# Performance work log

Measured on AMD Instinct MI355X. Metric: run time of the kernel, lower is better.

Reference implementation:

```python
import jax, jax.numpy as jnp
import numpy as np

B, T, TB, TV, TR = 4, 512, 512, 512, 256
D, H = 1024, 16
HD = D // H
D4 = D // 4
DFF = 4096
ROPE_THETA = 10000.0


def _rms(x, w, eps=1e-6):
    return x * jax.lax.rsqrt(jnp.mean(x * x, -1, keepdims=True) + eps) * w


def _ln(x, w, b, eps=1e-5):
    m = jnp.mean(x, -1, keepdims=True)
    v = jnp.var(x, -1, keepdims=True)
    return (x - m) * jax.lax.rsqrt(v + eps) * w + b


def _rope_cs(L, hd):
    inv = 1.0 / (ROPE_THETA ** (jnp.arange(0, hd, 2, dtype=jnp.float32) / hd))
    f = jnp.arange(L, dtype=jnp.float32)[:, None] * inv[None, :]
    e = jnp.concatenate([f, f], -1)  # (L, hd)
    return jnp.cos(e), jnp.sin(e)


def _rot_half(x):
    h = x.shape[-1] // 2
    return jnp.concatenate([-x[..., h:], x[..., :h]], -1)


def _rope(x, cos, sin):
    return x * cos + _rot_half(x) * sin


def _heads(x):
    b, l, _ = x.shape
    return x.reshape(b, l, H, HD).transpose(0, 2, 1, 3)  # (B,H,L,hd)


def setup_inputs() -> dict:
    key = jax.random.key(0)
    ks = jax.random.split(key, 16)
    def n(k, shape, s=0.02):
        return jax.random.normal(k, shape, jnp.float32) * s
    return {
        'x': n(ks[0], (B, T, D), 1.0),
        'bev_tokens': n(ks[1], (B, TB, D), 1.0),
        'vl_tokens': n(ks[2], (B, TV, D), 1.0),
        'reasoning_tokens': n(ks[3], (B, TR, D), 1.0),
        'conditioning': n(ks[4], (B, D), 1.0),
        'ln_pre_w': jnp.ones((D,)), 'ln_pre_b': jnp.zeros((D,)),
        'adaln_w': n(ks[5], (6 * D, D)), 'adaln_b': jnp.zeros((6 * D,)),
        'q_proj_w': n(ks[6], (D, D)), 'q_proj_b': jnp.zeros((D,)),
        'qa_w': n(ks[7], (3, D4, D)), 'qa_b': jnp.zeros((3, D4)),
        'qa_out_w': n(ks[8], (D, D4)), 'qa_out_b': jnp.zeros((D,)),
        'k_w': n(ks[9], (4, D, D)), 'k_b': jnp.zeros((4, D)),
        'v_w': n(ks[10], (4, D, D)), 'v_b': jnp.zeros((4, D)),
        'o_w': n(ks[11], (D, D)), 'o_b': jnp.zeros((D,)),
        'qn_w': jnp.ones((HD,)), 'kn_w': jnp.ones((HD,)),
        'gating': jnp.full((1,), 0.5, jnp.float32),
        'temps': jnp.zeros((4,)), 'score_biases': jnp.zeros((4,)),
        'ffn_ln_w': jnp.ones((D,)), 'ffn_ln_b': jnp.zeros((D,)),
        'ffn_w1': n(ks[12], (DFF, D)), 'ffn_b1': jnp.zeros((DFF,)),
        'ffn_w2': n(ks[13], (D, DFF)), 'ffn_b2': jnp.zeros((D,)),
    }


def reference(x, bev_tokens, vl_tokens, reasoning_tokens, conditioning,
              ln_pre_w, ln_pre_b, adaln_w, adaln_b,
              q_proj_w, q_proj_b, qa_w, qa_b, qa_out_w, qa_out_b,
              k_w, k_b, v_w, v_b, o_w, o_b, qn_w, kn_w,
              gating, temps, score_biases,
              ffn_ln_w, ffn_ln_b, ffn_w1, ffn_b1, ffn_w2, ffn_b2):
    # AdaLN modulation (T_route == 0 path: single modulation for whole sequence)
    mod = jax.nn.silu(conditioning) @ adaln_w.T + adaln_b  # (B, 6D)
    shift_pre, scale_pre, gate_attn, shift_ffn, scale_ffn, gate_ffn = jnp.split(mod, 6, axis=1)
    x_norm = _ln(x, ln_pre_w, ln_pre_b) * (1.0 + scale_pre[:, None, :]) + shift_pre[:, None, :]

    # Self Q and per-source K/V (sources: self, bev, vl, reasoning)
    q_self = _heads(x_norm @ q_proj_w.T + q_proj_b)
    srcs = [x_norm, bev_tokens, vl_tokens, reasoning_tokens]
    k_all = [_heads(s @ k_w[i].T + k_b[i]) for i, s in enumerate(srcs)]
    v_all = [_heads(s @ v_w[i].T + v_b[i]) for i, s in enumerate(srcs)]

    # Source-specific adapter queries: d -> d/4 -> d (shared out proj)
    q_ad = [_heads((x_norm @ qa_w[i].T + qa_b[i]) @ qa_out_w.T + qa_out_b) for i in range(3)]

    # QK-Norm (RMSNorm on head_dim)
    q_all = [_rms(q, qn_w) for q in [q_self] + q_ad]
    k_all = [_rms(k, kn_w) for k in k_all]

    # RoPE: Q and K for self-attention; K only for cross sources
    cosT, sinT = _rope_cs(x.shape[1], HD)
    q_all[0] = _rope(q_all[0], cosT, sinT)
    k_roped = []
    for k in k_all:
        c, s = _rope_cs(k.shape[2], HD)
        k_roped.append(_rope(k, c, s))

    # Per-source temperature / bias; gating only on reasoning scores
    temp = 1.0 + jax.nn.softplus(temps)
    ratio_g = jnp.tanh(gating[0])
    inv_sqrt_d = HD ** -0.5
    scores = []
    for i in range(4):
        s = jnp.einsum('bhqd,bhkd->bhqk', q_all[i], k_roped[i]) * (inv_sqrt_d * temp[i]) + score_biases[i]
        if i == 3:
            s = s * ratio_g
        scores.append(s)

    attn = jax.nn.softmax(jnp.concatenate(scores, -1), axis=-1)  # joint softmax
    v_cat = jnp.concatenate(v_all, 2)  # (B,H,T+TB+TV+TR,hd)
    out = jnp.einsum('bhqk,bhkd->bhqd', attn, v_cat)
    out = out.transpose(0, 2, 1, 3).reshape(x.shape) @ o_w.T + o_b
    x = x + gate_attn[:, None, :] * out

    # FFN with AdaLN modulation (dropout = identity at eval)
    h = _ln(x, ffn_ln_w, ffn_ln_b) * (1.0 + scale_ffn[:, None, :]) + shift_ffn[:, None, :]
    h = jax.nn.gelu(h @ ffn_w1.T + ffn_b1, approximate=False) @ ffn_w2.T + ffn_b2
    return x + gate_ffn[:, None, :] * h
```

## Files before the change

### kernel.cpp

```cpp
#include <hip/hip_runtime.h>

typedef unsigned short ushort_t;
typedef __attribute__((ext_vector_type(8))) __bf16 bf16x8;
typedef __attribute__((ext_vector_type(4))) float f32x4;

__device__ __forceinline__ float bf2f(ushort_t u) {
    union { unsigned int i; float f; } v; v.i = ((unsigned int)u) << 16; return v.f;
}
__device__ __forceinline__ ushort_t f2bf(float f) {
    union { float f; unsigned int i; } v; v.f = f;
    unsigned int r = (v.i + 0x7FFFu + ((v.i >> 16) & 1u)) >> 16;
    return (ushort_t)r;
}
__device__ __forceinline__ float gelu_exact(float v) {
    return 0.5f * v * (1.f + erff(v * 0.70710678118654752f));
}
__device__ __forceinline__ float ld1(const void* p, size_t i, int isf32) {
    return isf32 ? ((const float*)p)[i] : bf2f(((const ushort_t*)p)[i]);
}
__device__ __forceinline__ void stage8(const void* p, size_t idx, int isf32, ushort_t* dst) {
    if (isf32) {
        const float* f = (const float*)p + idx;
        float4 u = *(const float4*)f;
        float4 v = *(const float4*)(f + 4);
        dst[0] = f2bf(u.x); dst[1] = f2bf(u.y); dst[2] = f2bf(u.z); dst[3] = f2bf(u.w);
        dst[4] = f2bf(v.x); dst[5] = f2bf(v.y); dst[6] = f2bf(v.z); dst[7] = f2bf(v.w);
    } else {
        *(uint4*)dst = *(const uint4*)((const ushort_t*)p + idx);
    }
}
__device__ __forceinline__ void gload16(const ushort_t* g, ushort_t* l) {
    __builtin_amdgcn_global_load_lds(
        (const __attribute__((address_space(1))) unsigned int*)g,
        (__attribute__((address_space(3))) unsigned int*)l, 16, 0, 0);
}

__device__ __forceinline__ void store_q(ushort_t* qbuf, int row, int c, int p0, float v) {
    int b = row >> 9, t = row & 511;
    qbuf[((((size_t)(b * 16 + (c >> 6))) * 4 + p0) * 512 + t) * 64 + (c & 63)] = f2bf(v);
}
__device__ __forceinline__ void store_k(ushort_t* kbuf, int row, int c, int koff, int p1, float v) {
    int b = row >> p1, t = row & ((1 << p1) - 1);
    kbuf[(((size_t)(b * 16 + (c >> 6))) * 1792 + koff + t) * 64 + (c & 63)] = f2bf(v);
}
__device__ __forceinline__ void store_v(ushort_t* vbufT, int row, int c, int koff, int p1, float v) {
    int b = row >> p1, t = row & ((1 << p1) - 1);
    vbufT[(((size_t)(b * 16 + (c >> 6))) * 64 + (c & 63)) * 1792 + koff + t] = f2bf(v);
}

__global__ void detect_kernel(const unsigned int* __restrict__ x, int* __restrict__ flag) {
    if (threadIdx.x == 0 && blockIdx.x == 0) {
        int sane = 0;
        for (int i = 0; i < 256; i++) {
            unsigned int e = (x[i] >> 7) & 0xFFu;
            if (e == 0u || (e >= 100u && e <= 140u)) sane++;
        }
        *flag = (sane >= 200) ? 0 : 1;
    }
}

static constexpr size_t CV_ADALN = 0;
static constexpr size_t CV_QPROJ = 6291456;
static constexpr size_t CV_QA    = 7340032;
static constexpr size_t CV_QAOUT = 8126464;
static constexpr size_t CV_KW    = 8388608;
static constexpr size_t CV_VW    = 12582912;
static constexpr size_t CV_OW    = 16777216;
static constexpr size_t CV_FFN1  = 17825792;
static constexpr size_t CV_FFN2  = 22020096;
static constexpr size_t CV_TOTAL = 26214400;

__global__ void __launch_bounds__(256) convert_weights_kernel(
    const void* s0, const void* s1, const void* s2, const void* s3,
    const void* s4, const void* s5, const void* s6, const void* s7,
    const void* s8, ushort_t* __restrict__ dst, const int* __restrict__ dflag) {
    int isf32 = *dflag;
    size_t i8 = ((size_t)blockIdx.x * 256 + threadIdx.x) * 8;
    if (i8 >= CV_TOTAL) return;
    const void* src; size_t base;
    if      (i8 < CV_QPROJ) { src = s0; base = CV_ADALN; }
    else if (i8 < CV_QA)    { src = s1; base = CV_QPROJ; }
    else if (i8 < CV_QAOUT) { src = s2; base = CV_QA; }
    else if (i8 < CV_KW)    { src = s3; base = CV_QAOUT; }
    else if (i8 < CV_VW)    { src = s4; base = CV_KW; }
    else if (i8 < CV_OW)    { src = s5; base = CV_VW; }
    else if (i8 < CV_FFN1)  { src = s6; base = CV_OW; }
    else if (i8 < CV_FFN2)  { src = s7; base = CV_FFN1; }
    else                    { src = s8; base = CV_FFN2; }
    ushort_t t8[8];
    stage8(src, i8 - base, isf32, t8);
    *(uint4*)(dst + i8) = *(uint4*)t8;
}

__global__ void __launch_bounds__(256) convert_act_kernel(
    const void* __restrict__ src, ushort_t* __restrict__ dst, int n8,
    const int* __restrict__ dflag) {
    int c8 = blockIdx.x * 256 + threadIdx.x;
    if (c8 >= n8) return;
    int isf32 = *dflag;
    size_t i8 = (size_t)c8 * 8;
    ushort_t t8[8];
    stage8(src, i8, isf32, t8);
    *(uint4*)(dst + i8) = *(uint4*)t8;
}

__global__ void prep_consts_kernel(const void* __restrict__ temps,
                                   const void* __restrict__ biases,
                                   const void* __restrict__ gating,
                                   float* __restrict__ consts,
                                   const int* __restrict__ dflag) {
    if (threadIdx.x == 0 && blockIdx.x == 0) {
        int isf32 = *dflag;
        float g = tanhf(ld1(gating, 0, isf32));
        for (int s = 0; s < 4; s++) {
            float t  = ld1(temps, s, isf32);
            float sp = (t > 20.f) ? t : log1pf(expf(t));
            float scale = 0.125f * (1.f + sp);
            float mul = (s == 3) ? g : 1.f;
            consts[s]     = scale * mul;
            consts[4 + s] = ld1(biases, s, isf32) * mul;
        }
    }
}

__global__ void __launch_bounds__(256) adaln_kernel(
    const void* __restrict__ cond, const void* __restrict__ w,
    const void* __restrict__ bias, float* __restrict__ mod,
    int wmode, const int* __restrict__ dflag) {
    __shared__ float cs[1024];
    int isf32 = *dflag;
    int wf = (wmode == 2) ? 0 : isf32;
    int b = blockIdx.y, tid = threadIdx.x;
    for (int i = tid; i < 1024; i += 256) {
        float c = ld1(cond, b * 1024 + i, isf32);
        cs[i] = c / (1.f + expf(-c));
    }
    __syncthreads();
    int n = blockIdx.x * 256 + tid;
    float acc = 0.f;
    if (wf) {
        const float* wr = (const float*)w + (size_t)n * 1024;
        for (int d = 0; d < 1024; d += 8) {
            float4 a = *(const float4*)(wr + d);
            float4 bb = *(const float4*)(wr + d + 4);
            acc += cs[d+0]*a.x + cs[d+1]*a.y + cs[d+2]*a.z + cs[d+3]*a.w
                 + cs[d+4]*bb.x + cs[d+5]*bb.y + cs[d+6]*bb.z + cs[d+7]*bb.w;
        }
    } else {
        const ushort_t* wr = (const ushort_t*)w + (size_t)n * 1024;
        for (int d = 0; d < 1024; d += 8) {
            uint4 raw = *(const uint4*)(wr + d);
            const ushort_t* u = (const ushort_t*)&raw;
            acc += cs[d+0]*bf2f(u[0]) + cs[d+1]*bf2f(u[1]) + cs[d+2]*bf2f(u[2]) + cs[d+3]*bf2f(u[3])
                 + cs[d+4]*bf2f(u[4]) + cs[d+5]*bf2f(u[5]) + cs[d+6]*bf2f(u[6]) + cs[d+7]*bf2f(u[7]);
        }
    }
    mod[(size_t)b * 6144 + n] = acc + ld1(bias, n, isf32);
}

template <int SRC>
__global__ void __launch_bounds__(256) ln_mod_kernel(
    const void* __restrict__ xin, const float* __restrict__ mod,
    const void* __restrict__ lnw, const void* __restrict__ lnb,
    int shift_off, int scale_off, ushort_t* __restrict__ out,
    const int* __restrict__ dflag) {
    int isf32 = *dflag;
    int row = blockIdx.x, tid = threadIdx.x;
    int b = row >> 9;
    float v[4];
    #pragma unroll
    for (int i = 0; i < 4; i++) {
        size_t idx = (size_t)row * 1024 + tid + 256 * i;
        v[i] = (SRC == 1) ? ((const float*)xin)[idx] : ld1(xin, idx, isf32);
    }
    float s = v[0] + v[1] + v[2] + v[3];
    float ss = v[0]*v[0] + v[1]*v[1] + v[2]*v[2] + v[3]*v[3];
    #pragma unroll
    for (int off = 1; off < 64; off <<= 1) {
        s  += __shfl_xor(s,  off, 64);
        ss += __shfl_xor(ss, off, 64);
    }
    __shared__ float red[8];
    int w = tid >> 6;
    if ((tid & 63) == 0) { red[w] = s; red[4 + w] = ss; }
    __syncthreads();
    s  = red[0] + red[1] + red[2] + red[3];
    ss = red[4] + red[5] + red[6] + red[7];
    float mean = s * (1.f / 1024.f);
    float var  = ss * (1.f / 1024.f) - mean * mean;
    float inv  = rsqrtf(var + 1e-5f);
    const float* mb = mod + (size_t)b * 6144;
    #pragma unroll
    for (int i = 0; i < 4; i++) {
        int d = tid + 256 * i;
        float xn = (v[i] - mean) * inv;
        float y  = xn * ld1(lnw, d, isf32) + ld1(lnb, d, isf32);
        out[(size_t)row * 1024 + d] = f2bf(y * (1.f + mb[scale_off + d]) + mb[shift_off + d]);
    }
}

template <int EPI>
__global__ void __launch_bounds__(256) gemm_bt_kernel(
    const void* __restrict__ A, int lda,
    const void* __restrict__ W, int wrow0,
    const void* __restrict__ bias,
    void* __restrict__ Cout, int ldc, int K, int p0, int p1,
    int a_ext, int wmode, const int* __restrict__ dflag) {
    __shared__ ushort_t As[64][40];
    __shared__ ushort_t Bs[64][40];
    int isf32 = *dflag;
    int fa = a_ext ? isf32 : 0;
    int fw = (wmode == 2) ? 0 : isf32;
    int m0 = blockIdx.x * 64, n0 = blockIdx.y * 64;
    int tid = threadIdx.x;
    int r = tid >> 2, c = (tid & 3) * 8;
    int w = tid >> 6, ln = tid & 63;
    int msub = (w & 1) * 32, nsub = (w >> 1) * 32;
    int fr = ln & 15, q = ln >> 4;
    f32x4 acc00 = {0.f,0.f,0.f,0.f}, acc01 = {0.f,0.f,0.f,0.f};
    f32x4 acc10 = {0.f,0.f,0.f,0.f}, acc11 = {0.f,0.f,0.f,0.f};
    for (int k0 = 0; k0 < K; k0 += 32) {
        __syncthreads();
        {
            ushort_t t8[8];
            stage8(A, (size_t)(m0 + r) * lda + c + k0, fa, t8);
            *(uint4*)&As[r][c] = *(uint4*)t8;
        }
        {
            ushort_t t8[8];
            stage8(W, (size_t)(wrow0 + n0 + r) * K + c + k0, fw, t8);
            *(uint4*)&Bs[r][c] = *(uint4*)t8;
        }
        __syncthreads();
        bf16x8 a0 = *(const bf16x8*)&As[msub + fr][q * 8];
        bf16x8 a1 = *(const bf16x8*)&As[msub + 16 + fr][q * 8];
        bf16x8 b0 = *(const bf16x8*)&Bs[nsub + fr][q * 8];
        bf16x8 b1 = *(const bf16x8*)&Bs[nsub + 16 + fr][q * 8];
        acc00 = __builtin_amdgcn_mfma_f32_16x16x32_bf16(a0, b0, acc00, 0, 0, 0);
        acc01 = __builtin_amdgcn_mfma_f32_16x16x32_bf16(a0, b1, acc01, 0, 0, 0);
        acc10 = __builtin_amdgcn_mfma_f32_16x16x32_bf16(a1, b0, acc10, 0, 0, 0);
        acc11 = __builtin_amdgcn_mfma_f32_16x16x32_bf16(a1, b1, acc11, 0, 0, 0);
    }
    int col0 = n0 + nsub + fr;
    float bv0 = ld1(bias, wrow0 + col0, isf32);
    float bv1 = ld1(bias, wrow0 + col0 + 16, isf32);
    #pragma unroll
    for (int mi = 0; mi < 2; mi++) {
        #pragma unroll
        for (int ni = 0; ni < 2; ni++) {
            f32x4 a = (mi == 0) ? (ni == 0 ? acc00 : acc01) : (ni == 0 ? acc10 : acc11);
            int col = col0 + ni * 16;
            float bb = (ni == 0) ? bv0 : bv1;
            #pragma unroll
            for (int e = 0; e < 4; e++) {
                int rowg = m0 + msub + mi * 16 + q * 4 + e;
                float v = a[e] + bb;
                if (EPI == 2) v = gelu_exact(v);
                if (EPI == 0) {
                    ((float*)Cout)[(size_t)rowg * ldc + col] = v;
                } else if (EPI == 1 || EPI == 2) {
                    ((ushort_t*)Cout)[(size_t)rowg * ldc + col] = f2bf(v);
                } else if (EPI == 3) {
                    store_k((ushort_t*)Cout, rowg, col, p0, p1, v);
                } else if (EPI == 5) {
                    store_v((ushort_t*)Cout, rowg, col, p0, p1, v);
                } else {
                    store_q((ushort_t*)Cout, rowg, col, p0, v);
                }
            }
        }
    }
}

__device__ __forceinline__ void gemm_mainloop(
    const ushort_t* __restrict__ A, int lda,
    const ushort_t* __restrict__ W, int ldw,
    int m0, int wrow0, int kbeg, int klen,
    ushort_t* As, ushort_t* Bs, f32x4 acc[4][4])
{
    const int tid = threadIdx.x;
    const int w = tid >> 6;
    const int ln = tid & 63;
    const int fr = ln & 15, q = ln >> 4;
    const int wm = w & 1, wn = w >> 1;
    const ushort_t* gA = A + (size_t)(m0 + (tid >> 2)) * lda + kbeg + (tid & 3) * 8;
    const ushort_t* gW = W + (size_t)(wrow0 + (tid >> 2)) * ldw + kbeg + (tid & 3) * 8;
    const size_t sA = (size_t)64 * lda;
    const size_t sW = (size_t)64 * ldw;
    ushort_t* lA = As + w * 512;
    ushort_t* lB = Bs + w * 512;
    for (int k = 0; k < klen; k += 32) {
        __syncthreads();
        gload16(gA, lA);
        gload16(gA + sA, lA + 2048);
        gload16(gW, lB);
        gload16(gW + sW, lB + 2048);
        gA += 32; gW += 32;
        __syncthreads();
        bf16x8 af[4], bfr[4];
        #pragma unroll
        for (int mi = 0; mi < 4; mi++)
            af[mi] = *(const bf16x8*)&As[(wm * 64 + mi * 16 + fr) * 32 + q * 8];
        #pragma unroll
        for (int ni = 0; ni < 4; ni++)
            bfr[ni] = *(const bf16x8*)&Bs[(wn * 64 + ni * 16 + fr) * 32 + q * 8];
        #pragma unroll
        for (int mi = 0; mi < 4; mi++)
            #pragma unroll
            for (int ni = 0; ni < 4; ni++)
                acc[mi][ni] = __builtin_amdgcn_mfma_f32_16x16x32_bf16(af[mi], bfr[ni], acc[mi][ni], 0, 0, 0);
    }
}

__global__ void __launch_bounds__(256) gemm_qkvqa_kernel(
    const ushort_t* __restrict__ xnorm,
    const ushort_t* __restrict__ Wq, const ushort_t* __restrict__ Wqa,
    const ushort_t* __restrict__ Wk, const ushort_t* __restrict__ Wv,
    const void* __restrict__ bq, const void* __restrict__ bqa,
    const void* __restrict__ bk, const void* __restrict__ bv,
    ushort_t* __restrict__ qbuf, ushort_t* __restrict__ qah,
    ushort_t* __restrict__ kbuf, ushort_t* __restrict__ vbufT,
    const int* __restrict__ dflag)
{
    __shared__ ushort_t As[4096], Bs[4096];
    int isf32 = *dflag;
    int m0 = blockIdx.x * 128, n0 = blockIdx.y * 128;
    int seg, wrow0;
    const ushort_t* W; const void* bias;
    if (n0 < 1024)      { seg = 0; W = Wq;  bias = bq;  wrow0 = n0; }
    else if (n0 < 1792) { seg = 1; W = Wqa; bias = bqa; wrow0 = n0 - 1024; }
    else if (n0 < 2816) { seg = 2; W = Wk;  bias = bk;  wrow0 = n0 - 1792; }
    else                { seg = 3; W = Wv;  bias = bv;  wrow0 = n0 - 2816; }
    f32x4 acc[4][4];
    #pragma unroll
    for (int i = 0; i < 4; i++)
        #pragma unroll
        for (int j = 0; j < 4; j++) acc[i][j] = (f32x4){0.f, 0.f, 0.f, 0.f};
    gemm_mainloop(xnorm, 1024, W, 1024, m0, wrow0, 0, 1024, As, Bs, acc);
    int tid = threadIdx.x, w = tid >> 6, ln = tid & 63;
    int fr = ln & 15, q = ln >> 4, wm = w & 1, wn = w >> 1;
    #pragma unroll
    for (int ni = 0; ni < 4; ni++) {
        int c = wrow0 + wn * 64 + ni * 16 + fr;
        float bb = ld1(bias, c, isf32);
        #pragma unroll
        for (int mi = 0; mi < 4; mi++) {
            #pragma unroll
            for (int e = 0; e < 4; e++) {
                int row = m0 + wm * 64 + mi * 16 + q * 4 + e;
                float v = acc[mi][ni][e] + bb;
                if (seg == 0)      store_q(qbuf, row, c, 0, v);
                else if (seg == 1) qah[(size_t)row * 768 + c] = f2bf(v);
                else if (seg == 2) store_k(kbuf, row, c, 0, 9, v);
                else               store_v(vbufT, row, c, 0, 9, v);
            }
        }
    }
}

__global__ void __launch_bounds__(256) gemm_kv_kernel(
    const ushort_t* __restrict__ A,
    const ushort_t* __restrict__ Wk, const ushort_t* __restrict__ Wv,
    const void* __restrict__ kb, const void* __restrict__ vb, int boff,
    ushort_t* __restrict__ kbuf, ushort_t* __restrict__ vbufT,
    int koff, int p1, const int* __restrict__ dflag)
{
    __shared__ ushort_t As[4096], Bs[4096];
    int isf32 = *dflag;
    int m0 = blockIdx.x * 128, n0 = blockIdx.y * 128;
    int isK = (n0 < 1024);
    int wrow0 = isK ? n0 : n0 - 1024;
    const ushort_t* W = isK ? Wk : Wv;
    const void* bias = isK ? kb : vb;
    f32x4 acc[4][4];
    #pragma unroll
    for (int i = 0; i < 4; i++)
        #pragma unroll
        for (int j = 0; j < 4; j++) acc[i][j] = (f32x4){0.f, 0.f, 0.f, 0.f};
    gemm_mainloop(A, 1024, W, 1024, m0, wrow0, 0, 1024, As, Bs, acc);
    int tid = threadIdx.x, w = tid >> 6, ln = tid & 63;
    int fr = ln & 15, q = ln >> 4, wm = w & 1, wn = w >> 1;
    #pragma unroll
    for (int ni = 0; ni < 4; ni++) {
        int c = wrow0 + wn * 64 + ni * 16 + fr;
        float bb = ld1(bias, boff + c, isf32);
        #pragma unroll
        for (int mi = 0; mi < 4; mi++) {
            #pragma unroll
            for (int e = 0; e < 4; e++) {
                int row = m0 + wm * 64 + mi * 16 + q * 4 + e;
                float v = acc[mi][ni][e] + bb;
                if (isK) store_k(kbuf, row, c, koff, p1, v);
                else     store_v(vbufT, row, c, koff, p1, v);
            }
        }
    }
}

__global__ void __launch_bounds__(256) gemm_qaout_kernel(
    const ushort_t* __restrict__ qah,
    const ushort_t* __restrict__ W, const void* __restrict__ bias,
    ushort_t* __restrict__ qbuf, const int* __restrict__ dflag)
{
    __shared__ ushort_t As[4096], Bs[4096];
    int isf32 = *dflag;
    int m0 = blockIdx.x * 128, n0 = blockIdx.y * 128;
    int z = blockIdx.z;
    const ushort_t* A = qah + (size_t)z * 256;
    f32x4 acc[4][4];
    #pragma unroll
    for (int i = 0; i < 4; i++)
        #pragma unroll
        for (int j = 0; j < 4; j++) acc[i][j] = (f32x4){0.f, 0.f, 0.f, 0.f};
    gemm_mainloop(A, 768, W, 256, m0, n0, 0, 256, As, Bs, acc);
    int tid = threadIdx.x, w = tid >> 6, ln = tid & 63;
    int fr = ln & 15, q = ln >> 4, wm = w & 1, wn = w >> 1;
    #pragma unroll
    for (int ni = 0; ni < 4; ni++) {
        int c = n0 + wn * 64 + ni * 16 + fr;
        float bb = ld1(bias, c, isf32);
        #pragma unroll
        for (int mi = 0; mi < 4; mi++) {
            #pragma unroll
            for (int e = 0; e < 4; e++) {
                int row = m0 + wm * 64 + mi * 16 + q * 4 + e;
                store_q(qbuf, row, c, 1 + z, acc[mi][ni][e] + bb);
            }
        }
    }
}

template <int EPI>
__global__ void __launch_bounds__(256) gemm_plain_kernel(
    const ushort_t* __restrict__ A, int lda,
    const ushort_t* __restrict__ W, int ldw,
    const void* __restrict__ bias,
    void* __restrict__ Cout, int ldc, int ksub, size_t zstride,
    const int* __restrict__ dflag)
{
    __shared__ ushort_t As[4096], Bs[4096];
    int isf32 = *dflag;
    int m0 = blockIdx.x * 128, n0 = blockIdx.y * 128;
    int z = blockIdx.z;
    f32x4 acc[4][4];
    #pragma unroll
    for (int i = 0; i < 4; i++)
        #pragma unroll
        for (int j = 0; j < 4; j++) acc[i][j] = (f32x4){0.f, 0.f, 0.f, 0.f};
    gemm_mainloop(A, lda, W, ldw, m0, n0, z * ksub, ksub, As, Bs, acc);
    int tid = threadIdx.x, w = tid >> 6, ln = tid & 63;
    int fr = ln & 15, q = ln >> 4, wm = w & 1, wn = w >> 1;
    #pragma unroll
    for (int ni = 0; ni < 4; ni++) {
        int c = n0 + wn * 64 + ni * 16 + fr;
        float bb = (z == 0) ? ld1(bias, c, isf32) : 0.f;
        #pragma unroll
        for (int mi = 0; mi < 4; mi++) {
            #pragma unroll
            for (int e = 0; e < 4; e++) {
                int row = m0 + wm * 64 + mi * 16 + q * 4 + e;
                float v = acc[mi][ni][e] + bb;
                if (EPI == 2) {
                    ((ushort_t*)Cout)[(size_t)row * ldc + c] = f2bf(gelu_exact(v));
                } else {
                    ((float*)Cout)[z * zstride + (size_t)row * ldc + c] = v;
                }
            }
        }
    }
}

__global__ void __launch_bounds__(256) qrope_ip_kernel(
    ushort_t* __restrict__ qbuf, const void* __restrict__ qnw,
    const int* __restrict__ dflag) {
    int isf32 = *dflag;
    int w = threadIdx.x >> 6, ln = threadIdx.x & 63;
    int flat = blockIdx.x * 4 + w;
    int t = flat & 511, s = (flat >> 9) & 3;
    ushort_t* p = qbuf + (size_t)flat * 64;
    float x = bf2f(p[ln]);
    float ssum = x * x;
    #pragma unroll
    for (int off = 1; off < 64; off <<= 1) ssum += __shfl_xor(ssum, off, 64);
    float y = x * rsqrtf(ssum * (1.f / 64.f) + 1e-6f) * ld1(qnw, ln, isf32);
    if (s == 0) {
        float ang = (float)t * expf(-(float)(ln & 31) * (9.210340371976184f / 32.f));
        float cs, sn;
        sincosf(ang, &sn, &cs);
        float other = __shfl_xor(y, 32, 64);
        y = y * cs + ((ln < 32) ? -other : other) * sn;
    }
    p[ln] = f2bf(y);
}

__global__ void __launch_bounds__(256) krope_ip_kernel(
    ushort_t* __restrict__ kbuf, const void* __restrict__ knw,
    const int* __restrict__ dflag) {
    int isf32 = *dflag;
    int w = threadIdx.x >> 6, ln = threadIdx.x & 63;
    int flat = blockIdx.x * 4 + w;
    int j = flat % 1792;
    int t = j & 511;
    ushort_t* p = kbuf + (size_t)flat * 64;
    float x = bf2f(p[ln]);
    float ssum = x * x;
    #pragma unroll
    for (int off = 1; off < 64; off <<= 1) ssum += __shfl_xor(ssum, off, 64);
    float y = x * rsqrtf(ssum * (1.f / 64.f) + 1e-6f) * ld1(knw, ln, isf32);
    float ang = (float)t * expf(-(float)(ln & 31) * (9.210340371976184f / 32.f));
    float cs, sn;
    sincosf(ang, &sn, &cs);
    float other = __shfl_xor(y, 32, 64);
    y = y * cs + ((ln < 32) ? -other : other) * sn;
    p[ln] = f2bf(y);
}

__global__ void __launch_bounds__(256) attn_mfma_kernel(
    const ushort_t* __restrict__ qbuf, const ushort_t* __restrict__ kbuf,
    const ushort_t* __restrict__ vbufT, const float* __restrict__ consts,
    ushort_t* __restrict__ attn_out) {
    __shared__ ushort_t ks[2][64][72];
    __shared__ ushort_t vsT[2][64][72];
    __shared__ ushort_t ps[4][16][72];
    int bh = blockIdx.y;
    int b = bh >> 4, h = bh & 15;
    int tid = threadIdx.x, w = tid >> 6, ln = tid & 63;
    int r0 = blockIdx.x * 64 + w * 16;
    int m = ln & 15, quad = ln >> 4;

    const ushort_t* qb = qbuf + (size_t)bh * 4 * 512 * 64;
    bf16x8 qf00 = *(const bf16x8*)(qb + ((size_t)(0 * 512 + r0 + m)) * 64 + quad * 8);
    bf16x8 qf01 = *(const bf16x8*)(qb + ((size_t)(0 * 512 + r0 + m)) * 64 + 32 + quad * 8);
    bf16x8 qf10 = *(const bf16x8*)(qb + ((size_t)(1 * 512 + r0 + m)) * 64 + quad * 8);
    bf16x8 qf11 = *(const bf16x8*)(qb + ((size_t)(1 * 512 + r0 + m)) * 64 + 32 + quad * 8);
    bf16x8 qf20 = *(const bf16x8*)(qb + ((size_t)(2 * 512 + r0 + m)) * 64 + quad * 8);
    bf16x8 qf21 = *(const bf16x8*)(qb + ((size_t)(2 * 512 + r0 + m)) * 64 + 32 + quad * 8);
    bf16x8 qf30 = *(const bf16x8*)(qb + ((size_t)(3 * 512 + r0 + m)) * 64 + quad * 8);
    bf16x8 qf31 = *(const bf16x8*)(qb + ((size_t)(3 * 512 + r0 + m)) * 64 + 32 + quad * 8);

    float m_i[4], l_i[4];
    f32x4 acc[4];
    #pragma unroll
    for (int e = 0; e < 4; e++) { m_i[e] = -1e30f; l_i[e] = 0.f; }
    #pragma unroll
    for (int d = 0; d < 4; d++) acc[d] = (f32x4){0.f, 0.f, 0.f, 0.f};

    const ushort_t* kb  = kbuf  + (size_t)bh * 1792 * 64;
    const ushort_t* vbT = vbufT + (size_t)bh * 64 * 1792;
    int skey = tid >> 3, sd = (tid & 7) * 8;
    uint4 kreg0 = *(const uint4*)(kb + (size_t)skey * 64 + sd);
    uint4 kreg1 = *(const uint4*)(kb + (size_t)(skey + 32) * 64 + sd);
    uint4 vreg0 = *(const uint4*)(vbT + (size_t)skey * 1792 + sd);
    uint4 vreg1 = *(const uint4*)(vbT + (size_t)(skey + 32) * 1792 + sd);
    *(uint4*)&ks[0][skey][sd]       = kreg0;
    *(uint4*)&ks[0][skey + 32][sd]  = kreg1;
    *(uint4*)&vsT[0][skey][sd]      = vreg0;
    *(uint4*)&vsT[0][skey + 32][sd] = vreg1;
    __syncthreads();
    int tcnt = 0, p = 0;

    #pragma unroll
    for (int s = 0; s < 4; s++) {
        const float a_s = consts[s];
        const float b_s = consts[4 + s];
        const bf16x8 qA0 = (s == 0) ? qf00 : (s == 1) ? qf10 : (s == 2) ? qf20 : qf30;
        const bf16x8 qA1 = (s == 0) ? qf01 : (s == 1) ? qf11 : (s == 2) ? qf21 : qf31;
        const int NT = (s == 3) ? 4 : 8;
        for (int ti = 0; ti < NT; ti++) {
            if (tcnt < 27) {
                int nx = (tcnt + 1) * 64;
                kreg0 = *(const uint4*)(kb + (size_t)(nx + skey) * 64 + sd);
                kreg1 = *(const uint4*)(kb + (size_t)(nx + skey + 32) * 64 + sd);
                vreg0 = *(const uint4*)(vbT + (size_t)skey * 1792 + nx + sd);
                vreg1 = *(const uint4*)(vbT + (size_t)(skey + 32) * 1792 + nx + sd);
            }
            f32x4 zero = {0.f, 0.f, 0.f, 0.f};
            bf16x8 k0a = *(const bf16x8*)&ks[p][m][quad * 8];
            bf16x8 k0b = *(const bf16x8*)&ks[p][m][32 + quad * 8];
            bf16x8 k1a = *(const bf16x8*)&ks[p][16 + m][quad * 8];
            bf16x8 k1b = *(const bf16x8*)&ks[p][16 + m][32 + quad * 8];
            bf16x8 k2a = *(const bf16x8*)&ks[p][32 + m][quad * 8];
            bf16x8 k2b = *(const bf16x8*)&ks[p][32 + m][32 + quad * 8];
            bf16x8 k3a = *(const bf16x8*)&ks[p][48 + m][quad * 8];
            bf16x8 k3b = *(const bf16x8*)&ks[p][48 + m][32 + quad * 8];
            f32x4 sc0 = __builtin_amdgcn_mfma_f32_16x16x32_bf16(qA0, k0a, zero, 0, 0, 0);
            sc0 = __builtin_amdgcn_mfma_f32_16x16x32_bf16(qA1, k0b, sc0, 0, 0, 0);
            f32x4 sc1 = __builtin_amdgcn_mfma_f32_16x16x32_bf16(qA0, k1a, zero, 0, 0, 0);
            sc1 = __builtin_amdgcn_mfma_f32_16x16x32_bf16(qA1, k1b, sc1, 0, 0, 0);
            f32x4 sc2 = __builtin_amdgcn_mfma_f32_16x16x32_bf16(qA0, k2a, zero, 0, 0, 0);
            sc2 = __builtin_amdgcn_mfma_f32_16x16x32_bf16(qA1, k2b, sc2, 0, 0, 0);
            f32x4 sc3 = __builtin_amdgcn_mfma_f32_16x16x32_bf16(qA0, k3a, zero, 0, 0, 0);
            sc3 = __builtin_amdgcn_mfma_f32_16x16x32_bf16(qA1, k3b, sc3, 0, 0, 0);
            #pragma unroll
            for (int e = 0; e < 4; e++) {
                float s0 = sc0[e] * a_s + b_s;
                float s1 = sc1[e] * a_s + b_s;
                float s2 = sc2[e] * a_s + b_s;
                float s3 = sc3[e] * a_s + b_s;
                float mxe = fmaxf(fmaxf(s0, s1), fmaxf(s2, s3));
                #pragma unroll
                for (int off = 1; off < 16; off <<= 1) mxe = fmaxf(mxe, __shfl_xor(mxe, off, 64));
                float mnew = fmaxf(m_i[e], mxe);
                float p0 = __expf(s0 - mnew), p1 = __expf(s1 - mnew);
                float p2 = __expf(s2 - mnew), p3 = __expf(s3 - mnew);
                float rsum = (p0 + p1) + (p2 + p3);
                #pragma unroll
                for (int off = 1; off < 16; off <<= 1) rsum += __shfl_xor(rsum, off, 64);
                float alpha = __expf(m_i[e] - mnew);
                m_i[e] = mnew;
                l_i[e] = l_i[e] * alpha + rsum;
                acc[0][e] *= alpha; acc[1][e] *= alpha;
                acc[2][e] *= alpha; acc[3][e] *= alpha;
                int row = quad * 4 + e;
                ps[w][row][m]      = f2bf(p0);
                ps[w][row][m + 16] = f2bf(p1);
                ps[w][row][m + 32] = f2bf(p2);
                ps[w][row][m + 48] = f2bf(p3);
            }
            bf16x8 pA0 = *(const bf16x8*)&ps[w][m][quad * 8];
            bf16x8 pA1 = *(const bf16x8*)&ps[w][m][32 + quad * 8];
            #pragma unroll
            for (int dsub = 0; dsub < 4; dsub++) {
                bf16x8 vB0 = *(const bf16x8*)&vsT[p][dsub * 16 + m][quad * 8];
                bf16x8 vB1 = *(const bf16x8*)&vsT[p][dsub * 16 + m][32 + quad * 8];
                acc[dsub] = __builtin_amdgcn_mfma_f32_16x16x32_bf16(pA0, vB0, acc[dsub], 0, 0, 0);
                acc[dsub] = __builtin_amdgcn_mfma_f32_16x16x32_bf16(pA1, vB1, acc[dsub], 0, 0, 0);
            }
            if (tcnt < 27) {
                *(uint4*)&ks[1 - p][skey][sd]       = kreg0;
                *(uint4*)&ks[1 - p][skey + 32][sd]  = kreg1;
                *(uint4*)&vsT[1 - p][skey][sd]      = vreg0;
                *(uint4*)&vsT[1 - p][skey + 32][sd] = vreg1;
            }
            __syncthreads();
            p ^= 1;
            tcnt++;
        }
    }
    #pragma unroll
    for (int e = 0; e < 4; e++) {
        int t = r0 + quad * 4 + e;
        float invl = 1.f / l_i[e];
        #pragma unroll
        for (int dsub = 0; dsub < 4; dsub++) {
            int d = dsub * 16 + m;
            attn_out[(((size_t)(b * 512 + t)) * 16 + h) * 64 + d] = f2bf(acc[dsub][e] * invl);
        }
    }
}

__global__ void resgate_kernel(const void* __restrict__ x, const float* __restrict__ p0,
                               const float* __restrict__ p1,
                               const float* __restrict__ mod, float* __restrict__ x1,
                               int two, const int* __restrict__ dflag) {
    int isf32 = *dflag;
    int i = blockIdx.x * 256 + threadIdx.x;
    int b = i >> 19, n = i & 1023;
    float proj = p0[i] + (two ? p1[i] : 0.f);
    x1[i] = ld1(x, i, isf32) + mod[(size_t)b * 6144 + 2048 + n] * proj;
}
__global__ void final_kernel(const float* __restrict__ x1, const float* __restrict__ f0,
                             const float* __restrict__ f1,
                             const float* __restrict__ mod, void* __restrict__ out,
                             int two, const int* __restrict__ dflag) {
    int isf32 = *dflag;
    int i = blockIdx.x * 256 + threadIdx.x;
    int b = i >> 19, n = i & 1023;
    float ffn = f0[i] + (two ? f1[i] : 0.f);
    float val = x1[i] + mod[(size_t)b * 6144 + 5120 + n] * ffn;
    if (isf32) ((float*)out)[i] = val;
    else       ((ushort_t*)out)[i] = f2bf(val);
}

static constexpr size_t OFF_CONSTS   = 0;
static constexpr size_t OFF_FLAG     = 64;
static constexpr size_t OFF_MOD      = 512;
static constexpr size_t OFF_XNORM    = OFF_MOD    + 98304;
static constexpr size_t OFF_QAH      = OFF_XNORM  + 4194304;
static constexpr size_t OFF_KBUF     = OFF_XNORM  + 8388608;
static constexpr size_t OFF_VBUF     = OFF_KBUF   + 14680064;
static constexpr size_t OFF_QBUF     = OFF_VBUF   + 14680064;
static constexpr size_t OFF_ATTNOUT  = OFF_QBUF   + 16777216;
static constexpr size_t OFF_X1       = OFF_XNORM;
static constexpr size_t OFF_PROJ0    = OFF_QBUF;
static constexpr size_t OFF_PROJ1    = OFF_QBUF   + 8388608;
static constexpr size_t OFF_HMID     = OFF_KBUF;
static constexpr size_t OFF_HIN      = OFF_ATTNOUT;
static constexpr size_t OFF_ACT      = OFF_ATTNOUT;
static constexpr size_t OFF_WCACHE   = OFF_ATTNOUT + 4194304;
static constexpr size_t WS_NEED      = OFF_WCACHE + CV_TOTAL * 2;

extern "C" void kernel_launch(void* const* d_in, const int* in_sizes, int n_in,
                              void* d_out, int out_size, void* d_ws, size_t ws_size,
                              hipStream_t stream) {
    (void)in_sizes; (void)n_in; (void)out_size;
    const void* x        = d_in[0];
    const void* bev      = d_in[1];
    const void* vl       = d_in[2];
    const void* reas     = d_in[3];
    const void* cond     = d_in[4];
    const void* ln_pre_w = d_in[5];
    const void* ln_pre_b = d_in[6];
    const void* adaln_w  = d_in[7];
    const void* adaln_b  = d_in[8];
    const void* q_proj_w = d_in[9];
    const void* q_proj_b = d_in[10];
    const void* qa_w     = d_in[11];
    const void* qa_b     = d_in[12];
    const void* qa_out_w = d_in[13];
    const void* qa_out_b = d_in[14];
    const void* k_w      = d_in[15];
    const void* k_b      = d_in[16];
    const void* v_w      = d_in[17];
    const void* v_b      = d_in[18];
    const void* o_w      = d_in[19];
    const void* o_b      = d_in[20];
    const void* qn_w     = d_in[21];
    const void* kn_w     = d_in[22];
    const void* gating   = d_in[23];
    const void* temps    = d_in[24];
    const void* sbias    = d_in[25];
    const void* ffn_ln_w = d_in[26];
    const void* ffn_ln_b = d_in[27];
    const void* ffn_w1   = d_in[28];
    const void* ffn_b1   = d_in[29];
    const void* ffn_w2   = d_in[30];
    const void* ffn_b2   = d_in[31];

    char* ws = (char*)d_ws;
    float*    consts   = (float*)(ws + OFF_CONSTS);
    int*      dflag    = (int*)(ws + OFF_FLAG);
    float*    mod      = (float*)(ws + OFF_MOD);
    ushort_t* xnorm    = (ushort_t*)(ws + OFF_XNORM);
    ushort_t* qah      = (ushort_t*)(ws + OFF_QAH);
    ushort_t* kbuf     = (ushort_t*)(ws + OFF_KBUF);
    ushort_t* vbufT    = (ushort_t*)(ws + OFF_VBUF);
    ushort_t* qbuf     = (ushort_t*)(ws + OFF_QBUF);
    ushort_t* attnout  = (ushort_t*)(ws + OFF_ATTNOUT);
    float*    x1       = (float*)(ws + OFF_X1);
    float*    proj0    = (float*)(ws + OFF_PROJ0);
    float*    proj1    = (float*)(ws + OFF_PROJ1);
    ushort_t* hmid     = (ushort_t*)(ws + OFF_HMID);
    ushort_t* hin      = (ushort_t*)(ws + OFF_HIN);
    ushort_t* actbuf   = (ushort_t*)(ws + OFF_ACT);
    ushort_t* wc       = (ushort_t*)(ws + OFF_WCACHE);

    const bool use_cache = (ws_size >= WS_NEED);

    detect_kernel<<<1, 64, 0, stream>>>((const unsigned int*)x, dflag);
    prep_consts_kernel<<<1, 64, 0, stream>>>(temps, sbias, gating, consts, dflag);

    if (use_cache) {
        convert_weights_kernel<<<12800, 256, 0, stream>>>(
            adaln_w, q_proj_w, qa_w, qa_out_w, k_w, v_w, o_w, ffn_w1, ffn_w2, wc, dflag);
        adaln_kernel<<<dim3(24, 4), 256, 0, stream>>>(cond, wc + CV_ADALN, adaln_b, mod, 2, dflag);
        ln_mod_kernel<0><<<2048, 256, 0, stream>>>(x, mod, ln_pre_w, ln_pre_b, 0, 1024, xnorm, dflag);

        gemm_qkvqa_kernel<<<dim3(16, 30), 256, 0, stream>>>(
            xnorm, wc + CV_QPROJ, wc + CV_QA, wc + CV_KW, wc + CV_VW,
            q_proj_b, qa_b, k_b, v_b, qbuf, qah, kbuf, vbufT, dflag);
        gemm_qaout_kernel<<<dim3(16, 8, 3), 256, 0, stream>>>(
            qah, wc + CV_QAOUT, qa_out_b, qbuf, dflag);
        convert_act_kernel<<<1024, 256, 0, stream>>>(bev, actbuf, 262144, dflag);
        gemm_kv_kernel<<<dim3(16, 16), 256, 0, stream>>>(
            actbuf, wc + CV_KW + 1048576, wc + CV_VW + 1048576,
            k_b, v_b, 1024, kbuf, vbufT, 512, 9, dflag);
        convert_act_kernel<<<1024, 256, 0, stream>>>(vl, actbuf, 262144, dflag);
        gemm_kv_kernel<<<dim3(16, 16), 256, 0, stream>>>(
            actbuf, wc + CV_KW + 2097152, wc + CV_VW + 2097152,
            k_b, v_b, 2048, kbuf, vbufT, 1024, 9, dflag);
        convert_act_kernel<<<512, 256, 0, stream>>>(reas, actbuf, 131072, dflag);
        gemm_kv_kernel<<<dim3(8, 16), 256, 0, stream>>>(
            actbuf, wc + CV_KW + 3145728, wc + CV_VW + 3145728,
            k_b, v_b, 3072, kbuf, vbufT, 1536, 8, dflag);

        qrope_ip_kernel<<<32768, 256, 0, stream>>>(qbuf, qn_w, dflag);
        krope_ip_kernel<<<28672, 256, 0, stream>>>(kbuf, kn_w, dflag);
        attn_mfma_kernel<<<dim3(8, 64), 256, 0, stream>>>(qbuf, kbuf, vbufT, consts, attnout);

        gemm_plain_kernel<0><<<dim3(16, 8, 2), 256, 0, stream>>>(
            attnout, 1024, wc + CV_OW, 1024, o_b, proj0, 1024, 512, (size_t)2048 * 1024, dflag);
        resgate_kernel<<<8192, 256, 0, stream>>>(x, proj0, proj1, mod, x1, 1, dflag);
        ln_mod_kernel<1><<<2048, 256, 0, stream>>>(x1, mod, ffn_ln_w, ffn_ln_b, 3072, 4096, hin, dflag);
        gemm_plain_kernel<2><<<dim3(16, 32, 1), 256, 0, stream>>>(
            hin, 1024, wc + CV_FFN1, 1024, ffn_b1, hmid, 4096, 1024, 0, dflag);
        gemm_plain_kernel<0><<<dim3(16, 8, 2), 256, 0, stream>>>(
            hmid, 4096, wc + CV_FFN2, 4096, ffn_b2, proj0, 1024, 2048, (size_t)2048 * 1024, dflag);
        final_kernel<<<8192, 256, 0, stream>>>(x1, proj0, proj1, mod, d_out, 1, dflag);
    } else {
        adaln_kernel<<<dim3(24, 4), 256, 0, stream>>>(cond, adaln_w, adaln_b, mod, 0, dflag);
        ln_mod_kernel<0><<<2048, 256, 0, stream>>>(x, mod, ln_pre_w, ln_pre_b, 0, 1024, xnorm, dflag);
        gemm_bt_kernel<4><<<dim3(32, 16), 256, 0, stream>>>(xnorm, 1024, q_proj_w, 0, q_proj_b, qbuf, 0, 1024, 0, 9, 0, 0, dflag);
        {
            const void* srcs[4] = {xnorm, bev, vl, reas};
            const int koffs[4] = {0, 512, 1024, 1536};
            const int p1s[4]   = {9, 9, 9, 8};
            for (int i = 0; i < 4; i++) {
                int aext = (i == 0) ? 0 : 1;
                int gx = (i == 3) ? 16 : 32;
                gemm_bt_kernel<3><<<dim3(gx, 16), 256, 0, stream>>>(
                    srcs[i], 1024, k_w, i * 1024, k_b, kbuf, 0, 1024, koffs[i], p1s[i], aext, 0, dflag);
                gemm_bt_kernel<5><<<dim3(gx, 16), 256, 0, stream>>>(
                    srcs[i], 1024, v_w, i * 1024, v_b, vbufT, 0, 1024, koffs[i], p1s[i], aext, 0, dflag);
            }
        }
        gemm_bt_kernel<1><<<dim3(32, 12), 256, 0, stream>>>(xnorm, 1024, qa_w, 0, qa_b, qah, 768, 1024, 0, 0, 0, 0, dflag);
        for (int i = 0; i < 3; i++)
            gemm_bt_kernel<4><<<dim3(32, 16), 256, 0, stream>>>(qah + i * 256, 768, qa_out_w, 0, qa_out_b,
                                                                qbuf, 0, 256, 1 + i, 9, 0, 0, dflag);
        qrope_ip_kernel<<<32768, 256, 0, stream>>>(qbuf, qn_w, dflag);
        krope_ip_kernel<<<28672, 256, 0, stream>>>(kbuf, kn_w, dflag);
        attn_mfma_kernel<<<dim3(8, 64), 256, 0, stream>>>(qbuf, kbuf, vbufT, consts, attnout);
        gemm_bt_kernel<0><<<dim3(32, 16), 256, 0, stream>>>(attnout, 1024, o_w, 0, o_b, proj0, 1024, 1024, 0, 0, 0, 0, dflag);
        resgate_kernel<<<8192, 256, 0, stream>>>(x, proj0, proj0, mod, x1, 0, dflag);
        ln_mod_kernel<1><<<2048, 256, 0, stream>>>(x1, mod, ffn_ln_w, ffn_ln_b, 3072, 4096, hin, dflag);
        gemm_bt_kernel<2><<<dim3(32, 64), 256, 0, stream>>>(hin, 1024, ffn_w1, 0, ffn_b1, hmid, 4096, 1024, 0, 0, 0, 0, dflag);
        gemm_bt_kernel<0><<<dim3(32, 16), 256, 0, stream>>>(hmid, 4096, ffn_w2, 0, ffn_b2, proj0, 1024, 4096, 0, 0, 0, 0, dflag);
        final_kernel<<<8192, 256, 0, stream>>>(x1, proj0, proj0, mod, d_out, 0, dflag);
    }
}
```

Baseline: 615.2 us.

## Split attention over key halves, widen split-K, merge KV launches, drop adaLN conversion

Attention is split across two key ranges (blockIdx.z) with partial accumulators, row max and row sum, then merged by a new combine kernel. This doubles the number of blocks and adds a lazy-rescale threshold to the online softmax. The three BEV/VL/reasoning K/V GEMMs and their activation conversions are each fused into one launch. The O-projection and FFN2 GEMMs now use a 4-way split-K with separate output buffers, and the adaLN weights are no longer pre-converted to bf16. The changes aim to cut launch count and improve GPU occupancy, at the cost of extra fp32 partial traffic and a combine pass.

```diff
diff --git a/kernel.cpp b/kernel.cpp
--- a/kernel.cpp
+++ b/kernel.cpp
@@ -59,49 +59,55 @@
     }
 }
 
-static constexpr size_t CV_ADALN = 0;
-static constexpr size_t CV_QPROJ = 6291456;
-static constexpr size_t CV_QA    = 7340032;
-static constexpr size_t CV_QAOUT = 8126464;
-static constexpr size_t CV_KW    = 8388608;
-static constexpr size_t CV_VW    = 12582912;
-static constexpr size_t CV_OW    = 16777216;
-static constexpr size_t CV_FFN1  = 17825792;
-static constexpr size_t CV_FFN2  = 22020096;
-static constexpr size_t CV_TOTAL = 26214400;
+static constexpr size_t CW_QPROJ = 0;
+static constexpr size_t CW_QA    = 1048576;
+static constexpr size_t CW_QAOUT = 1835008;
+static constexpr size_t CW_KW    = 2097152;
+static constexpr size_t CW_VW    = 6291456;
+static constexpr size_t CW_OW    = 10485760;
+static constexpr size_t CW_FFN1  = 11534336;
+static constexpr size_t CW_FFN2  = 15728640;
+static constexpr size_t CW_TOTAL = 19922944;
 
 __global__ void __launch_bounds__(256) convert_weights_kernel(
     const void* s0, const void* s1, const void* s2, const void* s3,
     const void* s4, const void* s5, const void* s6, const void* s7,
-    const void* s8, ushort_t* __restrict__ dst, const int* __restrict__ dflag) {
+    ushort_t* __restrict__ dst, const int* __restrict__ dflag) {
     int isf32 = *dflag;
     size_t i8 = ((size_t)blockIdx.x * 256 + threadIdx.x) * 8;
-    if (i8 >= CV_TOTAL) return;
+    if (i8 >= CW_TOTAL) return;
     const void* src; size_t base;
-    if      (i8 < CV_QPROJ) { src = s0; base = CV_ADALN; }
-    else if (i8 < CV_QA)    { src = s1; base = CV_QPROJ; }
-    else if (i8 < CV_QAOUT) { src = s2; base = CV_QA; }
-    else if (i8 < CV_KW)    { src = s3; base = CV_QAOUT; }
-    else if (i8 < CV_VW)    { src = s4; base = CV_KW; }
-    else if (i8 < CV_OW)    { src = s5; base = CV_VW; }
-    else if (i8 < CV_FFN1)  { src = s6; base = CV_OW; }
-    else if (i8 < CV_FFN2)  { src = s7; base = CV_FFN1; }
-    else                    { src = s8; base = CV_FFN2; }
+    if      (i8 < CW_QA)    { src = s0; base = CW_QPROJ; }
+    else if (i8 < CW_QAOUT) { src = s1; base = CW_QA; }
+    else if (i8 < CW_KW)    { src = s2; base = CW_QAOUT; }
+    else if (i8 < CW_VW)    { src = s3; base = CW_KW; }
+    else if (i8 < CW_OW)    { src = s4; base = CW_VW; }
+    else if (i8 < CW_FFN1)  { src = s5; base = CW_OW; }
+    else if (i8 < CW_FFN2)  { src = s6; base = CW_FFN1; }
+    else                    { src = s7; base = CW_FFN2; }
     ushort_t t8[8];
     stage8(src, i8 - base, isf32, t8);
     *(uint4*)(dst + i8) = *(uint4*)t8;
 }
 
-__global__ void __launch_bounds__(256) convert_act_kernel(
-    const void* __restrict__ src, ushort_t* __restrict__ dst, int n8,
-    const int* __restrict__ dflag) {
-    int c8 = blockIdx.x * 256 + threadIdx.x;
-    if (c8 >= n8) return;
-    int isf32 = *dflag;
-    size_t i8 = (size_t)c8 * 8;
+__global__ void __launch_bounds__(256) convert_act3_kernel(
+    const void* __restrict__ bev, const void* __restrict__ vl,
+    const void* __restrict__ reas, ushort_t* __restrict__ actA,
+    ushort_t* __restrict__ actB, const int* __restrict__ dflag) {
+    int isf32 = *dflag;
+    size_t i8 = ((size_t)blockIdx.x * 256 + threadIdx.x) * 8;
+    if (i8 >= 5242880) return;
     ushort_t t8[8];
-    stage8(src, i8, isf32, t8);
-    *(uint4*)(dst + i8) = *(uint4*)t8;
+    if (i8 < 2097152) {
+        stage8(bev, i8, isf32, t8);
+        *(uint4*)(actA + i8) = *(uint4*)t8;
+    } else if (i8 < 4194304) {
+        stage8(vl, i8 - 2097152, isf32, t8);
+        *(uint4*)(actA + i8) = *(uint4*)t8;
+    } else {
+        stage8(reas, i8 - 4194304, isf32, t8);
+        *(uint4*)(actB + (i8 - 4194304)) = *(uint4*)t8;
+    }
 }
 
 __global__ void prep_consts_kernel(const void* __restrict__ temps,
@@ -358,26 +364,33 @@
     }
 }
 
-__global__ void __launch_bounds__(256) gemm_kv_kernel(
-    const ushort_t* __restrict__ A,
-    const ushort_t* __restrict__ Wk, const ushort_t* __restrict__ Wv,
-    const void* __restrict__ kb, const void* __restrict__ vb, int boff,
+__global__ void __launch_bounds__(256) gemm_kvx_kernel(
+    const ushort_t* __restrict__ actA, const ushort_t* __restrict__ actB,
+    const ushort_t* __restrict__ Wk1, const ushort_t* __restrict__ Wv1,
+    const void* __restrict__ kb_, const void* __restrict__ vb_,
     ushort_t* __restrict__ kbuf, ushort_t* __restrict__ vbufT,
-    int koff, int p1, const int* __restrict__ dflag)
+    const int* __restrict__ dflag)
 {
     __shared__ ushort_t As[4096], Bs[4096];
     int isf32 = *dflag;
-    int m0 = blockIdx.x * 128, n0 = blockIdx.y * 128;
+    int mb = blockIdx.x;
+    int src, koff, p1, srow0, am0;
+    const ushort_t* A;
+    if (mb < 16)      { src = 0; A = actA; am0 = mb * 128;        srow0 = mb * 128;        koff = 512;  p1 = 9; }
+    else if (mb < 32) { src = 1; A = actA; am0 = mb * 128;        srow0 = (mb - 16) * 128; koff = 1024; p1 = 9; }
+    else              { src = 2; A = actB; am0 = (mb - 32) * 128; srow0 = (mb - 32) * 128; koff = 1536; p1 = 8; }
+    int n0 = blockIdx.y * 128;
     int isK = (n0 < 1024);
     int wrow0 = isK ? n0 : n0 - 1024;
-    const ushort_t* W = isK ? Wk : Wv;
-    const void* bias = isK ? kb : vb;
+    const ushort_t* W = (isK ? Wk1 : Wv1) + (size_t)src * 1048576;
+    const void* bias = isK ? kb_ : vb_;
+    int boff = (src + 1) * 1024;
     f32x4 acc[4][4];
     #pragma unroll
     for (int i = 0; i < 4; i++)
         #pragma unroll
         for (int j = 0; j < 4; j++) acc[i][j] = (f32x4){0.f, 0.f, 0.f, 0.f};
-    gemm_mainloop(A, 1024, W, 1024, m0, wrow0, 0, 1024, As, Bs, acc);
+    gemm_mainloop(A, 1024, W, 1024, am0, wrow0, 0, 1024, As, Bs, acc);
     int tid = threadIdx.x, w = tid >> 6, ln = tid & 63;
     int fr = ln & 15, q = ln >> 4, wm = w & 1, wn = w >> 1;
     #pragma unroll
@@ -388,7 +401,7 @@
         for (int mi = 0; mi < 4; mi++) {
             #pragma unroll
             for (int e = 0; e < 4; e++) {
-                int row = m0 + wm * 64 + mi * 16 + q * 4 + e;
+                int row = srow0 + wm * 64 + mi * 16 + q * 4 + e;
                 float v = acc[mi][ni][e] + bb;
                 if (isK) store_k(kbuf, row, c, koff, p1, v);
                 else     store_v(vbufT, row, c, koff, p1, v);
@@ -435,13 +448,15 @@
     const ushort_t* __restrict__ A, int lda,
     const ushort_t* __restrict__ W, int ldw,
     const void* __restrict__ bias,
-    void* __restrict__ Cout, int ldc, int ksub, size_t zstride,
-    const int* __restrict__ dflag)
+    void* __restrict__ o0, void* __restrict__ o1,
+    void* __restrict__ o2, void* __restrict__ o3,
+    int ldc, int ksub, const int* __restrict__ dflag)
 {
     __shared__ ushort_t As[4096], Bs[4096];
     int isf32 = *dflag;
     int m0 = blockIdx.x * 128, n0 = blockIdx.y * 128;
     int z = blockIdx.z;
+    void* Cout = (z == 0) ? o0 : (z == 1) ? o1 : (z == 2) ? o2 : o3;
     f32x4 acc[4][4];
     #pragma unroll
     for (int i = 0; i < 4; i++)
@@ -463,7 +478,7 @@
                 if (EPI == 2) {
                     ((ushort_t*)Cout)[(size_t)row * ldc + c] = f2bf(gelu_exact(v));
                 } else {
-                    ((float*)Cout)[z * zstride + (size_t)row * ldc + c] = v;
+                    ((float*)Cout)[(size_t)row * ldc + c] = v;
                 }
             }
         }
@@ -484,7 +499,7 @@
     for (int off = 1; off < 64; off <<= 1) ssum += __shfl_xor(ssum, off, 64);
     float y = x * rsqrtf(ssum * (1.f / 64.f) + 1e-6f) * ld1(qnw, ln, isf32);
     if (s == 0) {
-        float ang = (float)t * expf(-(float)(ln & 31) * (9.210340371976184f / 32.f));
+        float ang = (float)t * __expf(-(float)(ln & 31) * (9.210340371976184f / 32.f));
         float cs, sn;
         sincosf(ang, &sn, &cs);
         float other = __shfl_xor(y, 32, 64);
@@ -507,7 +522,7 @@
     #pragma unroll
     for (int off = 1; off < 64; off <<= 1) ssum += __shfl_xor(ssum, off, 64);
     float y = x * rsqrtf(ssum * (1.f / 64.f) + 1e-6f) * ld1(knw, ln, isf32);
-    float ang = (float)t * expf(-(float)(ln & 31) * (9.210340371976184f / 32.f));
+    float ang = (float)t * __expf(-(float)(ln & 31) * (9.210340371976184f / 32.f));
     float cs, sn;
     sincosf(ang, &sn, &cs);
     float other = __shfl_xor(y, 32, 64);
@@ -516,6 +531,167 @@
 }
 
 __global__ void __launch_bounds__(256) attn_mfma_kernel(
+    const ushort_t* __restrict__ qbuf, const ushort_t* __restrict__ kbuf,
+    const ushort_t* __restrict__ vbufT, const float* __restrict__ consts,
+    float* __restrict__ pacc0, float* __restrict__ pacc1,
+    float* __restrict__ pml) {
+    __shared__ ushort_t ks[2][64][72];
+    __shared__ ushort_t vsT[2][64][72];
+    __shared__ ushort_t ps[4][16][72];
+    int bh = blockIdx.y;
+    int z = blockIdx.z;
+    int tid = threadIdx.x, w = tid >> 6, ln = tid & 63;
+    int r0 = blockIdx.x * 64 + w * 16;
+    int m = ln & 15, quad = ln >> 4;
+    const int ntile = z ? 12 : 16;
+    const int keybase = z * 1024;
+    const int s0i = z * 2;
+
+    const ushort_t* qb = qbuf + (size_t)bh * 4 * 512 * 64;
+    bf16x8 qA0f = *(const bf16x8*)(qb + ((size_t)(s0i * 512 + r0 + m)) * 64 + quad * 8);
+    bf16x8 qA1f = *(const bf16x8*)(qb + ((size_t)(s0i * 512 + r0 + m)) * 64 + 32 + quad * 8);
+    bf16x8 qB0f = *(const bf16x8*)(qb + ((size_t)((s0i + 1) * 512 + r0 + m)) * 64 + quad * 8);
+    bf16x8 qB1f = *(const bf16x8*)(qb + ((size_t)((s0i + 1) * 512 + r0 + m)) * 64 + 32 + quad * 8);
+
+    const float aA = consts[s0i],     bA = consts[4 + s0i];
+    const float aB = consts[s0i + 1], bB = consts[4 + s0i + 1];
+
+    float m_i[4], l_i[4];
+    f32x4 acc[4];
+    #pragma unroll
+    for (int e = 0; e < 4; e++) { m_i[e] = -1e30f; l_i[e] = 0.f; }
+    #pragma unroll
+    for (int d = 0; d < 4; d++) acc[d] = (f32x4){0.f, 0.f, 0.f, 0.f};
+
+    const ushort_t* kb  = kbuf  + (size_t)bh * 1792 * 64 + (size_t)keybase * 64;
+    const ushort_t* vbT = vbufT + (size_t)bh * 64 * 1792 + keybase;
+    int skey = tid >> 3, sd = (tid & 7) * 8;
+    uint4 kreg0 = *(const uint4*)(kb + (size_t)skey * 64 + sd);
+    uint4 kreg1 = *(const uint4*)(kb + (size_t)(skey + 32) * 64 + sd);
+    uint4 vreg0 = *(const uint4*)(vbT + (size_t)skey * 1792 + sd);
+    uint4 vreg1 = *(const uint4*)(vbT + (size_t)(skey + 32) * 1792 + sd);
+    *(uint4*)&ks[0][skey][sd]       = kreg0;
+    *(uint4*)&ks[0][skey + 32][sd]  = kreg1;
+    *(uint4*)&vsT[0][skey][sd]      = vreg0;
+    *(uint4*)&vsT[0][skey + 32][sd] = vreg1;
+    __syncthreads();
+    int p = 0;
+
+    for (int ti = 0; ti < ntile; ti++) {
+        if (ti + 1 < ntile) {
+            int nx = (ti + 1) * 64;
+            kreg0 = *(const uint4*)(kb + (size_t)(nx + skey) * 64 + sd);
+            kreg1 = *(const uint4*)(kb + (size_t)(nx + skey + 32) * 64 + sd);
+            vreg0 = *(const uint4*)(vbT + (size_t)skey * 1792 + nx + sd);
+            vreg1 = *(const uint4*)(vbT + (size_t)(skey + 32) * 1792 + nx + sd);
+        }
+        int sl = (ti >= 8) ? 1 : 0;
+        float a_s = sl ? aB : aA;
+        float b_s = sl ? bB : bA;
+        bf16x8 qA0 = sl ? qB0f : qA0f;
+        bf16x8 qA1 = sl ? qB1f : qA1f;
+        f32x4 zero = {0.f, 0.f, 0.f, 0.f};
+        bf16x8 k0a = *(const bf16x8*)&ks[p][m][quad * 8];
+        bf16x8 k0b = *(const bf16x8*)&ks[p][m][32 + quad * 8];
+        bf16x8 k1a = *(const bf16x8*)&ks[p][16 + m][quad * 8];
+        bf16x8 k1b = *(const bf16x8*)&ks[p][16 + m][32 + quad * 8];
+        bf16x8 k2a = *(const bf16x8*)&ks[p][32 + m][quad * 8];
+        bf16x8 k2b = *(const bf16x8*)&ks[p][32 + m][32 + quad * 8];
+        bf16x8 k3a = *(const bf16x8*)&ks[p][48 + m][quad * 8];
+        bf16x8 k3b = *(const bf16x8*)&ks[p][48 + m][32 + quad * 8];
+        f32x4 sc0 = __builtin_amdgcn_mfma_f32_16x16x32_bf16(qA0, k0a, zero, 0, 0, 0);
+        sc0 = __builtin_amdgcn_mfma_f32_16x16x32_bf16(qA1, k0b, sc0, 0, 0, 0);
+        f32x4 sc1 = __builtin_amdgcn_mfma_f32_16x16x32_bf16(qA0, k1a, zero, 0, 0, 0);
+        sc1 = __builtin_amdgcn_mfma_f32_16x16x32_bf16(qA1, k1b, sc1, 0, 0, 0);
+        f32x4 sc2 = __builtin_amdgcn_mfma_f32_16x16x32_bf16(qA0, k2a, zero, 0, 0, 0);
+        sc2 = __builtin_amdgcn_mfma_f32_16x16x32_bf16(qA1, k2b, sc2, 0, 0, 0);
+        f32x4 sc3 = __builtin_amdgcn_mfma_f32_16x16x32_bf16(qA0, k3a, zero, 0, 0, 0);
+        sc3 = __builtin_amdgcn_mfma_f32_16x16x32_bf16(qA1, k3b, sc3, 0, 0, 0);
+        #pragma unroll
+        for (int e = 0; e < 4; e++) {
+            float s0 = sc0[e] * a_s + b_s;
+            float s1 = sc1[e] * a_s + b_s;
+            float s2 = sc2[e] * a_s + b_s;
+            float s3 = sc3[e] * a_s + b_s;
+            float mxe = fmaxf(fmaxf(s0, s1), fmaxf(s2, s3));
+            #pragma unroll
+            for (int off = 1; off < 16; off <<= 1) mxe = fmaxf(mxe, __shfl_xor(mxe, off, 64));
+            if (mxe > m_i[e] + 8.f) {
+                float alpha = __expf(m_i[e] - mxe);
+                m_i[e] = mxe;
+                l_i[e] *= alpha;
+                acc[0][e] *= alpha; acc[1][e] *= alpha;
+                acc[2][e] *= alpha; acc[3][e] *= alpha;
+            }
+            float p0 = __expf(s0 - m_i[e]), p1 = __expf(s1 - m_i[e]);
+            float p2 = __expf(s2 - m_i[e]), p3 = __expf(s3 - m_i[e]);
+            l_i[e] += (p0 + p1) + (p2 + p3);
+            int row = quad * 4 + e;
+            ps[w][row][m]      = f2bf(p0);
+            ps[w][row][m + 16] = f2bf(p1);
+            ps[w][row][m + 32] = f2bf(p2);
+            ps[w][row][m + 48] = f2bf(p3);
+        }
+        bf16x8 pA0 = *(const bf16x8*)&ps[w][m][quad * 8];
+        bf16x8 pA1 = *(const bf16x8*)&ps[w][m][32 + quad * 8];
+        #pragma unroll
+        for (int dsub = 0; dsub < 4; dsub++) {
+            bf16x8 vB0 = *(const bf16x8*)&vsT[p][dsub * 16 + m][quad * 8];
+            bf16x8 vB1 = *(const bf16x8*)&vsT[p][dsub * 16 + m][32 + quad * 8];
+            acc[dsub] = __builtin_amdgcn_mfma_f32_16x16x32_bf16(pA0, vB0, acc[dsub], 0, 0, 0);
+            acc[dsub] = __builtin_amdgcn_mfma_f32_16x16x32_bf16(pA1, vB1, acc[dsub], 0, 0, 0);
+        }
+        if (ti + 1 < ntile) {
+            *(uint4*)&ks[1 - p][skey][sd]       = kreg0;
+            *(uint4*)&ks[1 - p][skey + 32][sd]  = kreg1;
+            *(uint4*)&vsT[1 - p][skey][sd]      = vreg0;
+            *(uint4*)&vsT[1 - p][skey + 32][sd] = vreg1;
+        }
+        __syncthreads();
+        p ^= 1;
+    }
+    #pragma unroll
+    for (int e = 0; e < 4; e++) {
+        float l = l_i[e];
+        #pragma unroll
+        for (int off = 1; off < 16; off <<= 1) l += __shfl_xor(l, off, 64);
+        l_i[e] = l;
+    }
+    float* pacc = z ? pacc1 : pacc0;
+    #pragma unroll
+    for (int e = 0; e < 4; e++) {
+        int t = r0 + quad * 4 + e;
+        if (m == 0) {
+            size_t mi = (((size_t)z * 64 + bh) * 512 + t) * 2;
+            pml[mi]     = m_i[e];
+            pml[mi + 1] = l_i[e];
+        }
+        #pragma unroll
+        for (int dsub = 0; dsub < 4; dsub++) {
+            pacc[((size_t)bh * 512 + t) * 64 + dsub * 16 + m] = acc[dsub][e];
+        }
+    }
+}
+
+__global__ void __launch_bounds__(256) attn_combine_kernel(
+    const float* __restrict__ pacc0, const float* __restrict__ pacc1,
+    const float* __restrict__ pml, ushort_t* __restrict__ attn_out) {
+    int tid = threadIdx.x, w = tid >> 6, ln = tid & 63;
+    int idx = blockIdx.x * 4 + w;
+    int bh = idx >> 9, t = idx & 511;
+    int b = bh >> 4, h = bh & 15;
+    size_t r = (size_t)bh * 512 + t;
+    float m0 = pml[r * 2],                 l0 = pml[r * 2 + 1];
+    float m1 = pml[((size_t)32768 + r) * 2], l1 = pml[((size_t)32768 + r) * 2 + 1];
+    float M = fmaxf(m0, m1);
+    float w0 = __expf(m0 - M), w1 = __expf(m1 - M);
+    float inv = 1.f / (l0 * w0 + l1 * w1);
+    float a0 = pacc0[r * 64 + ln];
+    float a1 = pacc1[r * 64 + ln];
+    attn_out[(((size_t)(b * 512 + t)) * 16 + h) * 64 + ln] = f2bf((a0 * w0 + a1 * w1) * inv);
+}
+
+__global__ void __launch_bounds__(256) attn_mfma_legacy_kernel(
     const ushort_t* __restrict__ qbuf, const ushort_t* __restrict__ kbuf,
     const ushort_t* __restrict__ vbufT, const float* __restrict__ consts,
     ushort_t* __restrict__ attn_out) {
@@ -527,24 +703,19 @@
     int tid = threadIdx.x, w = tid >> 6, ln = tid & 63;
     int r0 = blockIdx.x * 64 + w * 16;
     int m = ln & 15, quad = ln >> 4;
-
     const ushort_t* qb = qbuf + (size_t)bh * 4 * 512 * 64;
-    bf16x8 qf00 = *(const bf16x8*)(qb + ((size_t)(0 * 512 + r0 + m)) * 64 + quad * 8);
-    bf16x8 qf01 = *(const bf16x8*)(qb + ((size_t)(0 * 512 + r0 + m)) * 64 + 32 + quad * 8);
-    bf16x8 qf10 = *(const bf16x8*)(qb + ((size_t)(1 * 512 + r0 + m)) * 64 + quad * 8);
-    bf16x8 qf11 = *(const bf16x8*)(qb + ((size_t)(1 * 512 + r0 + m)) * 64 + 32 + quad * 8);
-    bf16x8 qf20 = *(const bf16x8*)(qb + ((size_t)(2 * 512 + r0 + m)) * 64 + quad * 8);
-    bf16x8 qf21 = *(const bf16x8*)(qb + ((size_t)(2 * 512 + r0 + m)) * 64 + 32 + quad * 8);
-    bf16x8 qf30 = *(const bf16x8*)(qb + ((size_t)(3 * 512 + r0 + m)) * 64 + quad * 8);
-    bf16x8 qf31 = *(const bf16x8*)(qb + ((size_t)(3 * 512 + r0 + m)) * 64 + 32 + quad * 8);
-
+    bf16x8 qf[4][2];
+    #pragma unroll
+    for (int s = 0; s < 4; s++) {
+        qf[s][0] = *(const bf16x8*)(qb + ((size_t)(s * 512 + r0 + m)) * 64 + quad * 8);
+        qf[s][1] = *(const bf16x8*)(qb + ((size_t)(s * 512 + r0 + m)) * 64 + 32 + quad * 8);
+    }
     float m_i[4], l_i[4];
     f32x4 acc[4];
     #pragma unroll
     for (int e = 0; e < 4; e++) { m_i[e] = -1e30f; l_i[e] = 0.f; }
     #pragma unroll
     for (int d = 0; d < 4; d++) acc[d] = (f32x4){0.f, 0.f, 0.f, 0.f};
-
     const ushort_t* kb  = kbuf  + (size_t)bh * 1792 * 64;
     const ushort_t* vbT = vbufT + (size_t)bh * 64 * 1792;
     int skey = tid >> 3, sd = (tid & 7) * 8;
@@ -558,13 +729,12 @@
     *(uint4*)&vsT[0][skey + 32][sd] = vreg1;
     __syncthreads();
     int tcnt = 0, p = 0;
-
     #pragma unroll
     for (int s = 0; s < 4; s++) {
         const float a_s = consts[s];
         const float b_s = consts[4 + s];
-        const bf16x8 qA0 = (s == 0) ? qf00 : (s == 1) ? qf10 : (s == 2) ? qf20 : qf30;
-        const bf16x8 qA1 = (s == 0) ? qf01 : (s == 1) ? qf11 : (s == 2) ? qf21 : qf31;
+        const bf16x8 qA0 = qf[s][0];
+        const bf16x8 qA1 = qf[s][1];
         const int NT = (s == 3) ? 4 : 8;
         for (int ti = 0; ti < NT; ti++) {
             if (tcnt < 27) {
@@ -600,17 +770,16 @@
                 float mxe = fmaxf(fmaxf(s0, s1), fmaxf(s2, s3));
                 #pragma unroll
                 for (int off = 1; off < 16; off <<= 1) mxe = fmaxf(mxe, __shfl_xor(mxe, off, 64));
-                float mnew = fmaxf(m_i[e], mxe);
-                float p0 = __expf(s0 - mnew), p1 = __expf(s1 - mnew);
-                float p2 = __expf(s2 - mnew), p3 = __expf(s3 - mnew);
-                float rsum = (p0 + p1) + (p2 + p3);
-                #pragma unroll
-                for (int off = 1; off < 16; off <<= 1) rsum += __shfl_xor(rsum, off, 64);
-                float alpha = __expf(m_i[e] - mnew);
-                m_i[e] = mnew;
-                l_i[e] = l_i[e] * alpha + rsum;
-                acc[0][e] *= alpha; acc[1][e] *= alpha;
-                acc[2][e] *= alpha; acc[3][e] *= alpha;
+                if (mxe > m_i[e] + 8.f) {
+                    float alpha = __expf(m_i[e] - mxe);
+                    m_i[e] = mxe;
+                    l_i[e] *= alpha;
+                    acc[0][e] *= alpha; acc[1][e] *= alpha;
+                    acc[2][e] *= alpha; acc[3][e] *= alpha;
+                }
+                float p0 = __expf(s0 - m_i[e]), p1 = __expf(s1 - m_i[e]);
+                float p2 = __expf(s2 - m_i[e]), p3 = __expf(s3 - m_i[e]);
+                l_i[e] += (p0 + p1) + (p2 + p3);
                 int row = quad * 4 + e;
                 ps[w][row][m]      = f2bf(p0);
                 ps[w][row][m + 16] = f2bf(p1);
@@ -639,8 +808,11 @@
     }
     #pragma unroll
     for (int e = 0; e < 4; e++) {
+        float l = l_i[e];
+        #pragma unroll
+        for (int off = 1; off < 16; off <<= 1) l += __shfl_xor(l, off, 64);
+        float invl = 1.f / l;
         int t = r0 + quad * 4 + e;
-        float invl = 1.f / l_i[e];
         #pragma unroll
         for (int dsub = 0; dsub < 4; dsub++) {
             int d = dsub * 16 + m;
@@ -650,23 +822,27 @@
 }
 
 __global__ void resgate_kernel(const void* __restrict__ x, const float* __restrict__ p0,
-                               const float* __restrict__ p1,
+                               const float* __restrict__ p1, const float* __restrict__ p2,
+                               const float* __restrict__ p3,
                                const float* __restrict__ mod, float* __restrict__ x1,
-                               int two, const int* __restrict__ dflag) {
+                               int sum4, const int* __restrict__ dflag) {
     int isf32 = *dflag;
     int i = blockIdx.x * 256 + threadIdx.x;
     int b = i >> 19, n = i & 1023;
-    float proj = p0[i] + (two ? p1[i] : 0.f);
+    float proj = p0[i];
+    if (sum4) proj += p1[i] + p2[i] + p3[i];
     x1[i] = ld1(x, i, isf32) + mod[(size_t)b * 6144 + 2048 + n] * proj;
 }
 __global__ void final_kernel(const float* __restrict__ x1, const float* __restrict__ f0,
-                             const float* __restrict__ f1,
+                             const float* __restrict__ f1, const float* __restrict__ f2,
+                             const float* __restrict__ f3,
                              const float* __restrict__ mod, void* __restrict__ out,
-                             int two, const int* __restrict__ dflag) {
+                             int sum4, const int* __restrict__ dflag) {
     int isf32 = *dflag;
     int i = blockIdx.x * 256 + threadIdx.x;
     int b = i >> 19, n = i & 1023;
-    float ffn = f0[i] + (two ? f1[i] : 0.f);
+    float ffn = f0[i];
+    if (sum4) ffn += f1[i] + f2[i] + f3[i];
     float val = x1[i] + mod[(size_t)b * 6144 + 5120 + n] * ffn;
     if (isf32) ((float*)out)[i] = val;
     else       ((ushort_t*)out)[i] = f2bf(val);
@@ -681,14 +857,10 @@
 static constexpr size_t OFF_VBUF     = OFF_KBUF   + 14680064;
 static constexpr size_t OFF_QBUF     = OFF_VBUF   + 14680064;
 static constexpr size_t OFF_ATTNOUT  = OFF_QBUF   + 16777216;
-static constexpr size_t OFF_X1       = OFF_XNORM;
-static constexpr size_t OFF_PROJ0    = OFF_QBUF;
-static constexpr size_t OFF_PROJ1    = OFF_QBUF   + 8388608;
-static constexpr size_t OFF_HMID     = OFF_KBUF;
-static constexpr size_t OFF_HIN      = OFF_ATTNOUT;
-static constexpr size_t OFF_ACT      = OFF_ATTNOUT;
 static constexpr size_t OFF_WCACHE   = OFF_ATTNOUT + 4194304;
-static constexpr size_t WS_NEED      = OFF_WCACHE + CV_TOTAL * 2;
+static constexpr size_t OFF_PACC1    = OFF_WCACHE + CW_TOTAL * 2;
+static constexpr size_t OFF_PML      = OFF_PACC1  + 8388608;
+static constexpr size_t WS_NEED      = OFF_WCACHE + 52428800;
 
 extern "C" void kernel_launch(void* const* d_in, const int* in_sizes, int n_in,
                               void* d_out, int out_size, void* d_ws, size_t ws_size,
@@ -737,13 +909,23 @@
     ushort_t* vbufT    = (ushort_t*)(ws + OFF_VBUF);
     ushort_t* qbuf     = (ushort_t*)(ws + OFF_QBUF);
     ushort_t* attnout  = (ushort_t*)(ws + OFF_ATTNOUT);
-    float*    x1       = (float*)(ws + OFF_X1);
-    float*    proj0    = (float*)(ws + OFF_PROJ0);
-    float*    proj1    = (float*)(ws + OFF_PROJ1);
-    ushort_t* hmid     = (ushort_t*)(ws + OFF_HMID);
-    ushort_t* hin      = (ushort_t*)(ws + OFF_HIN);
-    ushort_t* actbuf   = (ushort_t*)(ws + OFF_ACT);
+    float*    x1       = (float*)(ws + OFF_XNORM);
+    ushort_t* hmid     = (ushort_t*)(ws + OFF_KBUF);
+    ushort_t* hin      = (ushort_t*)(ws + OFF_ATTNOUT);
     ushort_t* wc       = (ushort_t*)(ws + OFF_WCACHE);
+    float*    pacc0    = (float*)(ws + OFF_XNORM);
+    float*    pacc1    = (float*)(ws + OFF_PACC1);
+    float*    pml      = (float*)(ws + OFF_PML);
+    ushort_t* actA     = (ushort_t*)(ws + OFF_PACC1);
+    ushort_t* actB     = (ushort_t*)(ws + OFF_ATTNOUT);
+    float*    op0      = (float*)(ws + OFF_KBUF);
+    float*    op1      = (float*)(ws + OFF_KBUF + 8388608);
+    float*    op2      = (float*)(ws + OFF_KBUF + 16777216);
+    float*    op3      = (float*)(ws + OFF_QBUF);
+    float*    f0       = (float*)(ws + OFF_QBUF);
+    float*    f1       = (float*)(ws + OFF_QBUF + 8388608);
+    float*    f2       = (float*)(ws + OFF_KBUF + 16777216);
+    float*    f3       = (float*)(ws + OFF_PACC1);
 
     const bool use_cache = (ws_size >= WS_NEED);
 
@@ -751,43 +933,38 @@
     prep_consts_kernel<<<1, 64, 0, stream>>>(temps, sbias, gating, consts, dflag);
 
     if (use_cache) {
-        convert_weights_kernel<<<12800, 256, 0, stream>>>(
-            adaln_w, q_proj_w, qa_w, qa_out_w, k_w, v_w, o_w, ffn_w1, ffn_w2, wc, dflag);
-        adaln_kernel<<<dim3(24, 4), 256, 0, stream>>>(cond, wc + CV_ADALN, adaln_b, mod, 2, dflag);
+        convert_weights_kernel<<<9728, 256, 0, stream>>>(
+            q_proj_w, qa_w, qa_out_w, k_w, v_w, o_w, ffn_w1, ffn_w2, wc, dflag);
+        convert_act3_kernel<<<2560, 256, 0, stream>>>(bev, vl, reas, actA, actB, dflag);
+        adaln_kernel<<<dim3(24, 4), 256, 0, stream>>>(cond, adaln_w, adaln_b, mod, 0, dflag);
         ln_mod_kernel<0><<<2048, 256, 0, stream>>>(x, mod, ln_pre_w, ln_pre_b, 0, 1024, xnorm, dflag);
 
         gemm_qkvqa_kernel<<<dim3(16, 30), 256, 0, stream>>>(
-            xnorm, wc + CV_QPROJ, wc + CV_QA, wc + CV_KW, wc + CV_VW,
+            xnorm, wc + CW_QPROJ, wc + CW_QA, wc + CW_KW, wc + CW_VW,
             q_proj_b, qa_b, k_b, v_b, qbuf, qah, kbuf, vbufT, dflag);
         gemm_qaout_kernel<<<dim3(16, 8, 3), 256, 0, stream>>>(
-            qah, wc + CV_QAOUT, qa_out_b, qbuf, dflag);
-        convert_act_kernel<<<1024, 256, 0, stream>>>(bev, actbuf, 262144, dflag);
-        gemm_kv_kernel<<<dim3(16, 16), 256, 0, stream>>>(
-            actbuf, wc + CV_KW + 1048576, wc + CV_VW + 1048576,
-            k_b, v_b, 1024, kbuf, vbufT, 512, 9, dflag);
-        convert_act_kernel<<<1024, 256, 0, stream>>>(vl, actbuf, 262144, dflag);
-        gemm_kv_kernel<<<dim3(16, 16), 256, 0, stream>>>(
-            actbuf, wc + CV_KW + 2097152, wc + CV_VW + 2097152,
-            k_b, v_b, 2048, kbuf, vbufT, 1024, 9, dflag);
-        convert_act_kernel<<<512, 256, 0, stream>>>(reas, actbuf, 131072, dflag);
-        gemm_kv_kernel<<<dim3(8, 16), 256, 0, stream>>>(
-            actbuf, wc + CV_KW + 3145728, wc + CV_VW + 3145728,
-            k_b, v_b, 3072, kbuf, vbufT, 1536, 8, dflag);
+            qah, wc + CW_QAOUT, qa_out_b, qbuf, dflag);
+        gemm_kvx_kernel<<<dim3(40, 16), 256, 0, stream>>>(
+            actA, actB, wc + CW_KW + 1048576, wc + CW_VW + 1048576,
+            k_b, v_b, kbuf, vbufT, dflag);
 
         qrope_ip_kernel<<<32768, 256, 0, stream>>>(qbuf, qn_w, dflag);
         krope_ip_kernel<<<28672, 256, 0, stream>>>(kbuf, kn_w, dflag);
-        attn_mfma_kernel<<<dim3(8, 64), 256, 0, stream>>>(qbuf, kbuf, vbufT, consts, attnout);
-
-        gemm_plain_kernel<0><<<dim3(16, 8, 2), 256, 0, stream>>>(
-            attnout, 1024, wc + CV_OW, 1024, o_b, proj0, 1024, 512, (size_t)2048 * 1024, dflag);
-        resgate_kernel<<<8192, 256, 0, stream>>>(x, proj0, proj1, mod, x1, 1, dflag);
+        attn_mfma_kernel<<<dim3(8, 64, 2), 256, 0, stream>>>(
+            qbuf, kbuf, vbufT, consts, pacc0, pacc1, pml);
+        attn_combine_kernel<<<8192, 256, 0, stream>>>(pacc0, pacc1, pml, attnout);
+
+        gemm_plain_kernel<0><<<dim3(16, 8, 4), 256, 0, stream>>>(
+            attnout, 1024, wc + CW_OW, 1024, o_b, op0, op1, op2, op3, 1024, 256, dflag);
+        resgate_kernel<<<8192, 256, 0, stream>>>(x, op0, op1, op2, op3, mod, x1, 1, dflag);
         ln_mod_kernel<1><<<2048, 256, 0, stream>>>(x1, mod, ffn_ln_w, ffn_ln_b, 3072, 4096, hin, dflag);
         gemm_plain_kernel<2><<<dim3(16, 32, 1), 256, 0, stream>>>(
-            hin, 1024, wc + CV_FFN1, 1024, ffn_b1, hmid, 4096, 1024, 0, dflag);
-        gemm_plain_kernel<0><<<dim3(16, 8, 2), 256, 0, stream>>>(
-            hmid, 4096, wc + CV_FFN2, 4096, ffn_b2, proj0, 1024, 2048, (size_t)2048 * 1024, dflag);
-        final_kernel<<<8192, 256, 0, stream>>>(x1, proj0, proj1, mod, d_out, 1, dflag);
+            hin, 1024, wc + CW_FFN1, 1024, ffn_b1, hmid, nullptr, nullptr, nullptr, 4096, 1024, dflag);
+        gemm_plain_kernel<0><<<dim3(16, 8, 4), 256, 0, stream>>>(
+            hmid, 4096, wc + CW_FFN2, 4096, ffn_b2, f0, f1, f2, f3, 1024, 1024, dflag);
+        final_kernel<<<8192, 256, 0, stream>>>(x1, f0, f1, f2, f3, mod, d_out, 1, dflag);
     } else {
+        float* proj0L = (float*)(ws + OFF_QBUF);
         adaln_kernel<<<dim3(24, 4), 256, 0, stream>>>(cond, adaln_w, adaln_b, mod, 0, dflag);
         ln_mod_kernel<0><<<2048, 256, 0, stream>>>(x, mod, ln_pre_w, ln_pre_b, 0, 1024, xnorm, dflag);
         gemm_bt_kernel<4><<<dim3(32, 16), 256, 0, stream>>>(xnorm, 1024, q_proj_w, 0, q_proj_b, qbuf, 0, 1024, 0, 9, 0, 0, dflag);
@@ -810,12 +987,12 @@
                                                                 qbuf, 0, 256, 1 + i, 9, 0, 0, dflag);
         qrope_ip_kernel<<<32768, 256, 0, stream>>>(qbuf, qn_w, dflag);
         krope_ip_kernel<<<28672, 256, 0, stream>>>(kbuf, kn_w, dflag);
-        attn_mfma_kernel<<<dim3(8, 64), 256, 0, stream>>>(qbuf, kbuf, vbufT, consts, attnout);
-        gemm_bt_kernel<0><<<dim3(32, 16), 256, 0, stream>>>(attnout, 1024, o_w, 0, o_b, proj0, 1024, 1024, 0, 0, 0, 0, dflag);
-        resgate_kernel<<<8192, 256, 0, stream>>>(x, proj0, proj0, mod, x1, 0, dflag);
+        attn_mfma_legacy_kernel<<<dim3(8, 64), 256, 0, stream>>>(qbuf, kbuf, vbufT, consts, attnout);
+        gemm_bt_kernel<0><<<dim3(32, 16), 256, 0, stream>>>(attnout, 1024, o_w, 0, o_b, proj0L, 1024, 1024, 0, 0, 0, 0, dflag);
+        resgate_kernel<<<8192, 256, 0, stream>>>(x, proj0L, proj0L, proj0L, proj0L, mod, x1, 0, dflag);
         ln_mod_kernel<1><<<2048, 256, 0, stream>>>(x1, mod, ffn_ln_w, ffn_ln_b, 3072, 4096, hin, dflag);
         gemm_bt_kernel<2><<<dim3(32, 64), 256, 0, stream>>>(hin, 1024, ffn_w1, 0, ffn_b1, hmid, 4096, 1024, 0, 0, 0, 0, dflag);
-        gemm_bt_kernel<0><<<dim3(32, 16), 256, 0, stream>>>(hmid, 4096, ffn_w2, 0, ffn_b2, proj0, 1024, 4096, 0, 0, 0, 0, dflag);
-        final_kernel<<<8192, 256, 0, stream>>>(x1, proj0, proj0, mod, d_out, 0, dflag);
-    }
-}
+        gemm_bt_kernel<0><<<dim3(32, 16), 256, 0, stream>>>(hmid, 4096, ffn_w2, 0, ffn_b2, proj0L, 1024, 4096, 0, 0, 0, 0, dflag);
+        final_kernel<<<8192, 256, 0, stream>>>(x1, proj0L, proj0L, proj0L, proj0L, mod, d_out, 0, dflag);
+    }
+}
```

Result: faster. 590.1 us (-4.1%).
